# Performance work log

Measured on AMD Instinct MI355X. Metric: run time of the kernel, lower is better.

Reference implementation:

```python
import jax, jax.numpy as jnp
import numpy as np


def setup_inputs() -> dict:
    key = jax.random.key(0)
    k1, k2 = jax.random.split(key)
    x = jax.random.normal(k1, (32, 112, 112, 64), dtype=jnp.float32)
    kernels = jax.random.normal(k2, (3, 3, 64, 128), dtype=jnp.float32) * 0.05
    biases = jnp.zeros((128,), dtype=jnp.float32)
    return {"x": x, "kernels": kernels, "biases": biases}


def reference(x, kernels, biases):
    # Stride-1 VALID cross-correlation, NHWC input, HWIO kernel -> NHWC output.
    # Matches the original's per-pixel sum(patch * kernel) over all input channels.
    out = jax.lax.conv_general_dilated(
        x, kernels,
        window_strides=(1, 1),
        padding="VALID",
        dimension_numbers=("NHWC", "HWIO", "NHWC"),
    )
    out = out + biases  # broadcast over (B, H_out, W_out, F)
    return jax.nn.relu(out)  # activation=relu per init_kwargs
```

## Files before the change

### kernel.cpp

```cpp
#include <hip/hip_runtime.h>
#include <hip/hip_bf16.h>

typedef __attribute__((ext_vector_type(4))) float f32x4;
typedef __attribute__((ext_vector_type(8))) short bf16x8;
typedef __attribute__((ext_vector_type(8))) unsigned short u16x8;
typedef __attribute__((ext_vector_type(4))) unsigned int u32x4;

#define HH 112
#define WW 112
#define CIN 64
#define COUT 128
#define HOUT 110
#define WOUT 110
#define MTOT 387200
#define NWG 3025
#define NXCD 8

__device__ __forceinline__ unsigned short f2bf(float f) {
  unsigned int x = __float_as_uint(f);
  x += 0x7fffu + ((x >> 16) & 1u);
  return (unsigned short)(x >> 16);
}

__device__ __forceinline__ unsigned int cvt2(float lo, float hi) {
  union { __hip_bfloat162 h; unsigned int u; } cv;
  cv.h = __float22bfloat162_rn(float2{lo, hi});
  return cv.u;
}

__global__ void prepack_b_kernel(const float* __restrict__ kern,
                                 unsigned short* __restrict__ bt) {
  int idx = blockIdx.x * 256 + threadIdx.x;
  if (idx >= 576 * COUT) return;
  int co = idx / 576;
  int k = idx - co * 576;
  bt[idx] = f2bf(kern[k * COUT + co]);
}

template <bool PREPACK>
__global__ __launch_bounds__(512)
void conv_mfma_kernel(const float* __restrict__ x,
                      const void* __restrict__ bsrc,
                      const float* __restrict__ bias,
                      float* __restrict__ out) {
  __shared__ __align__(16) unsigned short As[2][128 * 64];
  __shared__ __align__(16) unsigned short Bs[2][128 * 64];

  const int tid = threadIdx.x;

  const int bid = blockIdx.x;
  const int q = NWG / NXCD, r = NWG % NXCD;
  const int xcd = bid % NXCD, i8 = bid / NXCD;
  const int wg = (xcd < r ? xcd * (q + 1) : r * (q + 1) + (xcd - r) * q) + i8;
  const int m0 = wg * 128;

  const int sr = tid >> 2;
  const int sc = tid & 3;
  const int m = m0 + sr;
  const int wo = m % WOUT;
  const int t1 = m / WOUT;
  const int ho = t1 % HOUT;
  const int b = t1 / HOUT;
  const float* xrow = x + (((b * HH) + ho) * WW + wo) * CIN + sc * 16;
  const int swzS = (sr & 7) << 4;
  const int awoff0 = sr * 64 + ((((sc * 32) + 0) ^ swzS) >> 1);
  const int awoff1 = sr * 64 + ((((sc * 32) + 16) ^ swzS) >> 1);

  const unsigned short* btrow = nullptr;
  if constexpr (PREPACK) {
    btrow = (const unsigned short*)bsrc + sr * 576 + sc * 16;
  }
  const int bci = tid >> 3;
  const int bco = (tid & 7) * 16;

  const int lane = tid & 63;
  const int wid = tid >> 6;
  const int wm = wid >> 1;
  const int wn = wid & 1;
  const int l16 = lane & 15;
  const int lk = lane >> 4;
  const int swzR = (l16 & 7) << 4;

  const int aroff0 = (wm * 32 + 0 + l16) * 64;
  const int aroff1 = (wm * 32 + 16 + l16) * 64;
  const int broff0 = (wn * 64 + 0 + l16) * 64;
  const int broff1 = (wn * 64 + 16 + l16) * 64;
  const int broff2 = (wn * 64 + 32 + l16) * 64;
  const int broff3 = (wn * 64 + 48 + l16) * 64;

  f32x4 acc[2][4];
#pragma unroll
  for (int i = 0; i < 2; ++i)
#pragma unroll
    for (int j = 0; j < 4; ++j)
      acc[i][j] = (f32x4){0.f, 0.f, 0.f, 0.f};

  {
    f32x4 f0 = *(const f32x4*)(xrow + 0);
    f32x4 f1 = *(const f32x4*)(xrow + 4);
    f32x4 f2 = *(const f32x4*)(xrow + 8);
    f32x4 f3 = *(const f32x4*)(xrow + 12);
    u32x4 va, vb;
    va[0] = cvt2(f0[0], f0[1]); va[1] = cvt2(f0[2], f0[3]);
    va[2] = cvt2(f1[0], f1[1]); va[3] = cvt2(f1[2], f1[3]);
    vb[0] = cvt2(f2[0], f2[1]); vb[1] = cvt2(f2[2], f2[3]);
    vb[2] = cvt2(f3[0], f3[1]); vb[3] = cvt2(f3[2], f3[3]);
    *(u32x4*)(As[0] + awoff0) = va;
    *(u32x4*)(As[0] + awoff1) = vb;
    if constexpr (PREPACK) {
      const u16x8* p = (const u16x8*)btrow;
      *(u16x8*)(Bs[0] + awoff0) = p[0];
      *(u16x8*)(Bs[0] + awoff1) = p[1];
    } else {
      const float* kern = (const float*)bsrc;
      const float* kslab = kern + bci * COUT + bco;
      f32x4 g0 = *(const f32x4*)(kslab + 0);
      f32x4 g1 = *(const f32x4*)(kslab + 4);
      f32x4 g2 = *(const f32x4*)(kslab + 8);
      f32x4 g3 = *(const f32x4*)(kslab + 12);
#pragma unroll
      for (int j = 0; j < 4; ++j) {
        int c0 = bco + j;
        Bs[0][c0 * 64 + (((bci * 2) ^ ((c0 & 7) << 4)) >> 1)] = f2bf(g0[j]);
        int c1 = bco + 4 + j;
        Bs[0][c1 * 64 + (((bci * 2) ^ ((c1 & 7) << 4)) >> 1)] = f2bf(g1[j]);
        int c2 = bco + 8 + j;
        Bs[0][c2 * 64 + (((bci * 2) ^ ((c2 & 7) << 4)) >> 1)] = f2bf(g2[j]);
        int c3 = bco + 12 + j;
        Bs[0][c3 * 64 + (((bci * 2) ^ ((c3 & 7) << 4)) >> 1)] = f2bf(g3[j]);
      }
    }
  }

#pragma unroll
  for (int kk = 0; kk < 9; ++kk) {
    const int cur = kk & 1;
    const int nxt = cur ^ 1;

    f32x4 g0, g1, g2, g3;
    u16x8 bq0, bq1;
    if (kk < 8) {
      const int kn = kk + 1;
      const int kh2 = kn / 3;
      const int kw2 = kn - kh2 * 3;
      const float* src = xrow + (kh2 * WW + kw2) * CIN;
      g0 = *(const f32x4*)(src + 0);
      g1 = *(const f32x4*)(src + 4);
      g2 = *(const f32x4*)(src + 8);
      g3 = *(const f32x4*)(src + 12);
      if constexpr (PREPACK) {
        const u16x8* p = (const u16x8*)(btrow + kn * 64);
        bq0 = p[0];
        bq1 = p[1];
      }
    }

    __syncthreads();

    const unsigned short* Ac = As[cur];
    const unsigned short* Bc = Bs[cur];
#pragma unroll
    for (int ks = 0; ks < 2; ++ks) {
      const int cbs = ((ks * 64 + lk * 16) ^ swzR) >> 1;
      bf16x8 a0 = *(const bf16x8*)(Ac + aroff0 + cbs);
      bf16x8 a1 = *(const bf16x8*)(Ac + aroff1 + cbs);
      bf16x8 b0 = *(const bf16x8*)(Bc + broff0 + cbs);
      bf16x8 b1 = *(const bf16x8*)(Bc + broff1 + cbs);
      bf16x8 b2 = *(const bf16x8*)(Bc + broff2 + cbs);
      bf16x8 b3 = *(const bf16x8*)(Bc + broff3 + cbs);
      acc[0][0] = __builtin_amdgcn_mfma_f32_16x16x32_bf16(a0, b0, acc[0][0], 0, 0, 0);
      acc[0][1] = __builtin_amdgcn_mfma_f32_16x16x32_bf16(a0, b1, acc[0][1], 0, 0, 0);
      acc[0][2] = __builtin_amdgcn_mfma_f32_16x16x32_bf16(a0, b2, acc[0][2], 0, 0, 0);
      acc[0][3] = __builtin_amdgcn_mfma_f32_16x16x32_bf16(a0, b3, acc[0][3], 0, 0, 0);
      acc[1][0] = __builtin_amdgcn_mfma_f32_16x16x32_bf16(a1, b0, acc[1][0], 0, 0, 0);
      acc[1][1] = __builtin_amdgcn_mfma_f32_16x16x32_bf16(a1, b1, acc[1][1], 0, 0, 0);
      acc[1][2] = __builtin_amdgcn_mfma_f32_16x16x32_bf16(a1, b2, acc[1][2], 0, 0, 0);
      acc[1][3] = __builtin_amdgcn_mfma_f32_16x16x32_bf16(a1, b3, acc[1][3], 0, 0, 0);
    }

    if (kk < 8) {
      u32x4 va, vb;
      va[0] = cvt2(g0[0], g0[1]); va[1] = cvt2(g0[2], g0[3]);
      va[2] = cvt2(g1[0], g1[1]); va[3] = cvt2(g1[2], g1[3]);
      vb[0] = cvt2(g2[0], g2[1]); vb[1] = cvt2(g2[2], g2[3]);
      vb[2] = cvt2(g3[0], g3[1]); vb[3] = cvt2(g3[2], g3[3]);
      *(u32x4*)(As[nxt] + awoff0) = va;
      *(u32x4*)(As[nxt] + awoff1) = vb;
      if constexpr (PREPACK) {
        *(u16x8*)(Bs[nxt] + awoff0) = bq0;
        *(u16x8*)(Bs[nxt] + awoff1) = bq1;
      } else {
        const float* kern = (const float*)bsrc;
        const float* kslab = kern + ((kk + 1) * 64 + bci) * COUT + bco;
        f32x4 h0 = *(const f32x4*)(kslab + 0);
        f32x4 h1 = *(const f32x4*)(kslab + 4);
        f32x4 h2 = *(const f32x4*)(kslab + 8);
        f32x4 h3 = *(const f32x4*)(kslab + 12);
#pragma unroll
        for (int j = 0; j < 4; ++j) {
          int c0 = bco + j;
          Bs[nxt][c0 * 64 + (((bci * 2) ^ ((c0 & 7) << 4)) >> 1)] = f2bf(h0[j]);
          int c1 = bco + 4 + j;
          Bs[nxt][c1 * 64 + (((bci * 2) ^ ((c1 & 7) << 4)) >> 1)] = f2bf(h1[j]);
          int c2 = bco + 8 + j;
          Bs[nxt][c2 * 64 + (((bci * 2) ^ ((c2 & 7) << 4)) >> 1)] = f2bf(h2[j]);
          int c3 = bco + 12 + j;
          Bs[nxt][c3 * 64 + (((bci * 2) ^ ((c3 & 7) << 4)) >> 1)] = f2bf(h3[j]);
        }
      }
    }
  }

  const int ncol = wn * 64 + l16;
  const float bv0 = bias[ncol + 0];
  const float bv1 = bias[ncol + 16];
  const float bv2 = bias[ncol + 32];
  const float bv3 = bias[ncol + 48];
  const int mrow0 = m0 + wm * 32 + lk * 4;
#pragma unroll
  for (int mf = 0; mf < 2; ++mf) {
#pragma unroll
    for (int j = 0; j < 4; ++j) {
      const int row = mrow0 + mf * 16 + j;
      float* orow = out + (size_t)row * COUT + ncol;
      orow[0]  = fmaxf(acc[mf][0][j] + bv0, 0.f);
      orow[16] = fmaxf(acc[mf][1][j] + bv1, 0.f);
      orow[32] = fmaxf(acc[mf][2][j] + bv2, 0.f);
      orow[48] = fmaxf(acc[mf][3][j] + bv3, 0.f);
    }
  }
}

extern "C" void kernel_launch(void* const* d_in, const int* in_sizes, int n_in,
                              void* d_out, int out_size, void* d_ws, size_t ws_size,
                              hipStream_t stream) {
  const float* x = (const float*)d_in[0];
  const float* kern = (const float*)d_in[1];
  const float* bias = (const float*)d_in[2];
  float* out = (float*)d_out;

  const size_t bt_bytes = 576 * COUT * sizeof(unsigned short);
  if (d_ws != nullptr && ws_size >= bt_bytes) {
    unsigned short* bt = (unsigned short*)d_ws;
    prepack_b_kernel<<<288, 256, 0, stream>>>(kern, bt);
    conv_mfma_kernel<true><<<NWG, 512, 0, stream>>>(x, (const void*)bt, bias, out);
  } else {
    conv_mfma_kernel<false><<<NWG, 512, 0, stream>>>(x, (const void*)kern, bias, out);
  }
}
```

Baseline: 118.1 us.

## Load A fragments directly from global into registers, drop A LDS staging

The im2col A operand no longer goes through shared memory. Each lane loads its MFMA fragment rows straight from global fp32 input, converts them to bf16 in registers, and prefetches the next tap. The weight prepack now writes into the already-swizzled LDS layout per tap, so staging B is a linear copy, and launch bounds request 4 blocks per CU. This removes LDS writes and reads for A and halves shared-memory use to raise occupancy, at the cost of redundant global loads, since the two waves sharing wm load the same A rows, and higher register pressure.

```diff
diff --git a/kernel.cpp b/kernel.cpp
--- a/kernel.cpp
+++ b/kernel.cpp
@@ -31,20 +31,22 @@
 __global__ void prepack_b_kernel(const float* __restrict__ kern,
                                  unsigned short* __restrict__ bt) {
   int idx = blockIdx.x * 256 + threadIdx.x;
-  if (idx >= 576 * COUT) return;
-  int co = idx / 576;
-  int k = idx - co * 576;
-  bt[idx] = f2bf(kern[k * COUT + co]);
+  if (idx >= 9 * 8192) return;
+  int tap = idx >> 13;
+  int rem = idx & 8191;
+  int co = rem >> 6;
+  int e = rem & 63;
+  int ci = ((e * 2) ^ ((co & 7) << 4)) >> 1;
+  bt[idx] = f2bf(kern[(tap * 64 + ci) * COUT + co]);
 }
 
 template <bool PREPACK>
-__global__ __launch_bounds__(512)
+__global__ __launch_bounds__(512, 4)
 void conv_mfma_kernel(const float* __restrict__ x,
                       const void* __restrict__ bsrc,
                       const float* __restrict__ bias,
                       float* __restrict__ out) {
-  __shared__ __align__(16) unsigned short As[2][128 * 64];
-  __shared__ __align__(16) unsigned short Bs[2][128 * 64];
+  __shared__ __align__(16) unsigned short Bs[2][8192];
 
   const int tid = threadIdx.x;
 
@@ -53,25 +55,6 @@
   const int xcd = bid % NXCD, i8 = bid / NXCD;
   const int wg = (xcd < r ? xcd * (q + 1) : r * (q + 1) + (xcd - r) * q) + i8;
   const int m0 = wg * 128;
-
-  const int sr = tid >> 2;
-  const int sc = tid & 3;
-  const int m = m0 + sr;
-  const int wo = m % WOUT;
-  const int t1 = m / WOUT;
-  const int ho = t1 % HOUT;
-  const int b = t1 / HOUT;
-  const float* xrow = x + (((b * HH) + ho) * WW + wo) * CIN + sc * 16;
-  const int swzS = (sr & 7) << 4;
-  const int awoff0 = sr * 64 + ((((sc * 32) + 0) ^ swzS) >> 1);
-  const int awoff1 = sr * 64 + ((((sc * 32) + 16) ^ swzS) >> 1);
-
-  const unsigned short* btrow = nullptr;
-  if constexpr (PREPACK) {
-    btrow = (const unsigned short*)bsrc + sr * 576 + sc * 16;
-  }
-  const int bci = tid >> 3;
-  const int bco = (tid & 7) * 16;
 
   const int lane = tid & 63;
   const int wid = tid >> 6;
@@ -81,8 +64,21 @@
   const int lk = lane >> 4;
   const int swzR = (l16 & 7) << 4;
 
-  const int aroff0 = (wm * 32 + 0 + l16) * 64;
-  const int aroff1 = (wm * 32 + 16 + l16) * 64;
+  const float* pa[2];
+#pragma unroll
+  for (int f = 0; f < 2; ++f) {
+    const int mrow = m0 + wm * 32 + f * 16 + l16;
+    const int wo = mrow % WOUT;
+    const int t = mrow / WOUT;
+    const int ho = t % HOUT;
+    const int bb = t / HOUT;
+    pa[f] = x + (((bb * HH) + ho) * WW + wo) * CIN + lk * 8;
+  }
+
+  const unsigned short* btp = (const unsigned short*)bsrc;
+  const int bci = tid >> 3;
+  const int bco = (tid & 7) * 16;
+
   const int broff0 = (wn * 64 + 0 + l16) * 64;
   const int broff1 = (wn * 64 + 16 + l16) * 64;
   const int broff2 = (wn * 64 + 32 + l16) * 64;
@@ -95,40 +91,27 @@
     for (int j = 0; j < 4; ++j)
       acc[i][j] = (f32x4){0.f, 0.f, 0.f, 0.f};
 
-  {
-    f32x4 f0 = *(const f32x4*)(xrow + 0);
-    f32x4 f1 = *(const f32x4*)(xrow + 4);
-    f32x4 f2 = *(const f32x4*)(xrow + 8);
-    f32x4 f3 = *(const f32x4*)(xrow + 12);
-    u32x4 va, vb;
-    va[0] = cvt2(f0[0], f0[1]); va[1] = cvt2(f0[2], f0[3]);
-    va[2] = cvt2(f1[0], f1[1]); va[3] = cvt2(f1[2], f1[3]);
-    vb[0] = cvt2(f2[0], f2[1]); vb[1] = cvt2(f2[2], f2[3]);
-    vb[2] = cvt2(f3[0], f3[1]); vb[3] = cvt2(f3[2], f3[3]);
-    *(u32x4*)(As[0] + awoff0) = va;
-    *(u32x4*)(As[0] + awoff1) = vb;
-    if constexpr (PREPACK) {
-      const u16x8* p = (const u16x8*)btrow;
-      *(u16x8*)(Bs[0] + awoff0) = p[0];
-      *(u16x8*)(Bs[0] + awoff1) = p[1];
-    } else {
-      const float* kern = (const float*)bsrc;
-      const float* kslab = kern + bci * COUT + bco;
-      f32x4 g0 = *(const f32x4*)(kslab + 0);
-      f32x4 g1 = *(const f32x4*)(kslab + 4);
-      f32x4 g2 = *(const f32x4*)(kslab + 8);
-      f32x4 g3 = *(const f32x4*)(kslab + 12);
-#pragma unroll
-      for (int j = 0; j < 4; ++j) {
-        int c0 = bco + j;
-        Bs[0][c0 * 64 + (((bci * 2) ^ ((c0 & 7) << 4)) >> 1)] = f2bf(g0[j]);
-        int c1 = bco + 4 + j;
-        Bs[0][c1 * 64 + (((bci * 2) ^ ((c1 & 7) << 4)) >> 1)] = f2bf(g1[j]);
-        int c2 = bco + 8 + j;
-        Bs[0][c2 * 64 + (((bci * 2) ^ ((c2 & 7) << 4)) >> 1)] = f2bf(g2[j]);
-        int c3 = bco + 12 + j;
-        Bs[0][c3 * 64 + (((bci * 2) ^ ((c3 & 7) << 4)) >> 1)] = f2bf(g3[j]);
-      }
+  f32x4 p[2][2][2];
+  u16x8 bq0, bq1;
+
+#pragma unroll
+  for (int f = 0; f < 2; ++f)
+#pragma unroll
+    for (int ks = 0; ks < 2; ++ks)
+#pragma unroll
+      for (int h = 0; h < 2; ++h)
+        p[f][ks][h] = *(const f32x4*)(pa[f] + ks * 32 + h * 4);
+  if constexpr (PREPACK) {
+    const u16x8* s = (const u16x8*)(btp + tid * 16);
+    *(u16x8*)(Bs[0] + tid * 16) = s[0];
+    *(u16x8*)(Bs[0] + tid * 16 + 8) = s[1];
+  } else {
+    const float* kern = (const float*)bsrc;
+    const float* kslab = kern + bci * COUT + bco;
+#pragma unroll
+    for (int j = 0; j < 16; ++j) {
+      int c = bco + j;
+      Bs[0][c * 64 + (((bci * 2) ^ ((c & 7) << 4)) >> 1)] = f2bf(kslab[j]);
     }
   }
 
@@ -137,75 +120,69 @@
     const int cur = kk & 1;
     const int nxt = cur ^ 1;
 
-    f32x4 g0, g1, g2, g3;
-    u16x8 bq0, bq1;
+    __syncthreads();
+
+    bf16x8 af[2][2];
+#pragma unroll
+    for (int f = 0; f < 2; ++f)
+#pragma unroll
+      for (int ks = 0; ks < 2; ++ks) {
+        union { u32x4 u; bf16x8 b; } cv;
+        cv.u[0] = cvt2(p[f][ks][0][0], p[f][ks][0][1]);
+        cv.u[1] = cvt2(p[f][ks][0][2], p[f][ks][0][3]);
+        cv.u[2] = cvt2(p[f][ks][1][0], p[f][ks][1][1]);
+        cv.u[3] = cvt2(p[f][ks][1][2], p[f][ks][1][3]);
+        af[f][ks] = cv.b;
+      }
+
     if (kk < 8) {
       const int kn = kk + 1;
       const int kh2 = kn / 3;
       const int kw2 = kn - kh2 * 3;
-      const float* src = xrow + (kh2 * WW + kw2) * CIN;
-      g0 = *(const f32x4*)(src + 0);
-      g1 = *(const f32x4*)(src + 4);
-      g2 = *(const f32x4*)(src + 8);
-      g3 = *(const f32x4*)(src + 12);
+      const int off = (kh2 * WW + kw2) * CIN;
+#pragma unroll
+      for (int f = 0; f < 2; ++f)
+#pragma unroll
+        for (int ks = 0; ks < 2; ++ks)
+#pragma unroll
+          for (int h = 0; h < 2; ++h)
+            p[f][ks][h] = *(const f32x4*)(pa[f] + off + ks * 32 + h * 4);
       if constexpr (PREPACK) {
-        const u16x8* p = (const u16x8*)(btrow + kn * 64);
-        bq0 = p[0];
-        bq1 = p[1];
+        const u16x8* s = (const u16x8*)(btp + kn * 8192 + tid * 16);
+        bq0 = s[0];
+        bq1 = s[1];
       }
     }
 
-    __syncthreads();
-
-    const unsigned short* Ac = As[cur];
     const unsigned short* Bc = Bs[cur];
 #pragma unroll
     for (int ks = 0; ks < 2; ++ks) {
       const int cbs = ((ks * 64 + lk * 16) ^ swzR) >> 1;
-      bf16x8 a0 = *(const bf16x8*)(Ac + aroff0 + cbs);
-      bf16x8 a1 = *(const bf16x8*)(Ac + aroff1 + cbs);
       bf16x8 b0 = *(const bf16x8*)(Bc + broff0 + cbs);
       bf16x8 b1 = *(const bf16x8*)(Bc + broff1 + cbs);
       bf16x8 b2 = *(const bf16x8*)(Bc + broff2 + cbs);
       bf16x8 b3 = *(const bf16x8*)(Bc + broff3 + cbs);
-      acc[0][0] = __builtin_amdgcn_mfma_f32_16x16x32_bf16(a0, b0, acc[0][0], 0, 0, 0);
-      acc[0][1] = __builtin_amdgcn_mfma_f32_16x16x32_bf16(a0, b1, acc[0][1], 0, 0, 0);
-      acc[0][2] = __builtin_amdgcn_mfma_f32_16x16x32_bf16(a0, b2, acc[0][2], 0, 0, 0);
-      acc[0][3] = __builtin_amdgcn_mfma_f32_16x16x32_bf16(a0, b3, acc[0][3], 0, 0, 0);
-      acc[1][0] = __builtin_amdgcn_mfma_f32_16x16x32_bf16(a1, b0, acc[1][0], 0, 0, 0);
-      acc[1][1] = __builtin_amdgcn_mfma_f32_16x16x32_bf16(a1, b1, acc[1][1], 0, 0, 0);
-      acc[1][2] = __builtin_amdgcn_mfma_f32_16x16x32_bf16(a1, b2, acc[1][2], 0, 0, 0);
-      acc[1][3] = __builtin_amdgcn_mfma_f32_16x16x32_bf16(a1, b3, acc[1][3], 0, 0, 0);
+      acc[0][0] = __builtin_amdgcn_mfma_f32_16x16x32_bf16(af[0][ks], b0, acc[0][0], 0, 0, 0);
+      acc[0][1] = __builtin_amdgcn_mfma_f32_16x16x32_bf16(af[0][ks], b1, acc[0][1], 0, 0, 0);
+      acc[0][2] = __builtin_amdgcn_mfma_f32_16x16x32_bf16(af[0][ks], b2, acc[0][2], 0, 0, 0);
+      acc[0][3] = __builtin_amdgcn_mfma_f32_16x16x32_bf16(af[0][ks], b3, acc[0][3], 0, 0, 0);
+      acc[1][0] = __builtin_amdgcn_mfma_f32_16x16x32_bf16(af[1][ks], b0, acc[1][0], 0, 0, 0);
+      acc[1][1] = __builtin_amdgcn_mfma_f32_16x16x32_bf16(af[1][ks], b1, acc[1][1], 0, 0, 0);
+      acc[1][2] = __builtin_amdgcn_mfma_f32_16x16x32_bf16(af[1][ks], b2, acc[1][2], 0, 0, 0);
+      acc[1][3] = __builtin_amdgcn_mfma_f32_16x16x32_bf16(af[1][ks], b3, acc[1][3], 0, 0, 0);
     }
 
     if (kk < 8) {
-      u32x4 va, vb;
-      va[0] = cvt2(g0[0], g0[1]); va[1] = cvt2(g0[2], g0[3]);
-      va[2] = cvt2(g1[0], g1[1]); va[3] = cvt2(g1[2], g1[3]);
-      vb[0] = cvt2(g2[0], g2[1]); vb[1] = cvt2(g2[2], g2[3]);
-      vb[2] = cvt2(g3[0], g3[1]); vb[3] = cvt2(g3[2], g3[3]);
-      *(u32x4*)(As[nxt] + awoff0) = va;
-      *(u32x4*)(As[nxt] + awoff1) = vb;
       if constexpr (PREPACK) {
-        *(u16x8*)(Bs[nxt] + awoff0) = bq0;
-        *(u16x8*)(Bs[nxt] + awoff1) = bq1;
+        *(u16x8*)(Bs[nxt] + tid * 16) = bq0;
+        *(u16x8*)(Bs[nxt] + tid * 16 + 8) = bq1;
       } else {
         const float* kern = (const float*)bsrc;
         const float* kslab = kern + ((kk + 1) * 64 + bci) * COUT + bco;
-        f32x4 h0 = *(const f32x4*)(kslab + 0);
-        f32x4 h1 = *(const f32x4*)(kslab + 4);
-        f32x4 h2 = *(const f32x4*)(kslab + 8);
-        f32x4 h3 = *(const f32x4*)(kslab + 12);
-#pragma unroll
-        for (int j = 0; j < 4; ++j) {
-          int c0 = bco + j;
-          Bs[nxt][c0 * 64 + (((bci * 2) ^ ((c0 & 7) << 4)) >> 1)] = f2bf(h0[j]);
-          int c1 = bco + 4 + j;
-          Bs[nxt][c1 * 64 + (((bci * 2) ^ ((c1 & 7) << 4)) >> 1)] = f2bf(h1[j]);
-          int c2 = bco + 8 + j;
-          Bs[nxt][c2 * 64 + (((bci * 2) ^ ((c2 & 7) << 4)) >> 1)] = f2bf(h2[j]);
-          int c3 = bco + 12 + j;
-          Bs[nxt][c3 * 64 + (((bci * 2) ^ ((c3 & 7) << 4)) >> 1)] = f2bf(h3[j]);
+#pragma unroll
+        for (int j = 0; j < 16; ++j) {
+          int c = bco + j;
+          Bs[nxt][c * 64 + (((bci * 2) ^ ((c & 7) << 4)) >> 1)] = f2bf(kslab[j]);
         }
       }
     }
@@ -239,7 +216,7 @@
   const float* bias = (const float*)d_in[2];
   float* out = (float*)d_out;
 
-  const size_t bt_bytes = 576 * COUT * sizeof(unsigned short);
+  const size_t bt_bytes = 9 * 8192 * sizeof(unsigned short);
   if (d_ws != nullptr && ws_size >= bt_bytes) {
     unsigned short* bt = (unsigned short*)d_ws;
     prepack_b_kernel<<<288, 256, 0, stream>>>(kern, bt);
```

New measurement: 229.6 us. 1.94x slower.

## Pre-convert input to bf16 and stream tiles into LDS via direct global-to-LDS loads

Applied to the files above, without the earlier changes.

Adds a pre-pass that converts the whole fp32 input to bf16 in workspace. It also prepacks weights per tap in the pre-swizzled LDS layout. The main conv kernel then fills A and B tiles with global_load_lds 16-byte DMA, which removes the register staging and the in-loop conversion, and drops one barrier per tap. The cost is an extra full read and write of the input (about 150MB of traffic) before the conv, which may outweigh the saved in-kernel work. It also requires a larger workspace; otherwise the code falls back to the old path.

```diff
diff --git a/kernel.cpp b/kernel.cpp
--- a/kernel.cpp
+++ b/kernel.cpp
@@ -15,6 +15,7 @@
 #define MTOT 387200
 #define NWG 3025
 #define NXCD 8
+#define XNE 25690112
 
 __device__ __forceinline__ unsigned short f2bf(float f) {
   unsigned int x = __float_as_uint(f);
@@ -28,25 +29,46 @@
   return cv.u;
 }
 
+__device__ __forceinline__ void gload16(const unsigned short* g, unsigned short* l) {
+  __builtin_amdgcn_global_load_lds(
+      (const __attribute__((address_space(1))) void*)g,
+      (__attribute__((address_space(3))) void*)l, 16, 0, 0);
+}
+
+__global__ __launch_bounds__(256)
+void cvt_x_kernel(const float* __restrict__ x, unsigned short* __restrict__ xb) {
+  const int t = blockIdx.x * 256 + threadIdx.x;
+  const f32x4* s = (const f32x4*)x + (size_t)t * 2;
+  f32x4 a = s[0], b = s[1];
+  u32x4 v;
+  v[0] = cvt2(a[0], a[1]); v[1] = cvt2(a[2], a[3]);
+  v[2] = cvt2(b[0], b[1]); v[3] = cvt2(b[2], b[3]);
+  ((u32x4*)xb)[t] = v;
+}
+
 __global__ void prepack_b_kernel(const float* __restrict__ kern,
                                  unsigned short* __restrict__ bt) {
   int idx = blockIdx.x * 256 + threadIdx.x;
-  if (idx >= 576 * COUT) return;
-  int co = idx / 576;
-  int k = idx - co * 576;
-  bt[idx] = f2bf(kern[k * COUT + co]);
-}
-
-template <bool PREPACK>
-__global__ __launch_bounds__(512)
-void conv_mfma_kernel(const float* __restrict__ x,
-                      const void* __restrict__ bsrc,
-                      const float* __restrict__ bias,
-                      float* __restrict__ out) {
-  __shared__ __align__(16) unsigned short As[2][128 * 64];
-  __shared__ __align__(16) unsigned short Bs[2][128 * 64];
+  if (idx >= 9 * 8192) return;
+  int tap = idx >> 13;
+  int rem = idx & 8191;
+  int co = rem >> 6;
+  int e = rem & 63;
+  int ci = ((e * 2) ^ ((co & 7) << 4)) >> 1;
+  bt[idx] = f2bf(kern[(tap * 64 + ci) * COUT + co]);
+}
+
+__global__ __launch_bounds__(512, 4)
+void conv_dma_kernel(const unsigned short* __restrict__ xb,
+                     const unsigned short* __restrict__ bt,
+                     const float* __restrict__ bias,
+                     float* __restrict__ out) {
+  __shared__ __align__(16) unsigned short As[2][8192];
+  __shared__ __align__(16) unsigned short Bs[2][8192];
 
   const int tid = threadIdx.x;
+  const int lane = tid & 63;
+  const int wid = tid >> 6;
 
   const int bid = blockIdx.x;
   const int q = NWG / NXCD, r = NWG % NXCD;
@@ -54,27 +76,26 @@
   const int wg = (xcd < r ? xcd * (q + 1) : r * (q + 1) + (xcd - r) * q) + i8;
   const int m0 = wg * 128;
 
-  const int sr = tid >> 2;
-  const int sc = tid & 3;
-  const int m = m0 + sr;
-  const int wo = m % WOUT;
-  const int t1 = m / WOUT;
-  const int ho = t1 % HOUT;
-  const int b = t1 / HOUT;
-  const float* xrow = x + (((b * HH) + ho) * WW + wo) * CIN + sc * 16;
-  const int swzS = (sr & 7) << 4;
-  const int awoff0 = sr * 64 + ((((sc * 32) + 0) ^ swzS) >> 1);
-  const int awoff1 = sr * 64 + ((((sc * 32) + 16) ^ swzS) >> 1);
-
-  const unsigned short* btrow = nullptr;
-  if constexpr (PREPACK) {
-    btrow = (const unsigned short*)bsrc + sr * 576 + sc * 16;
-  }
-  const int bci = tid >> 3;
-  const int bco = (tid & 7) * 16;
-
-  const int lane = tid & 63;
-  const int wid = tid >> 6;
+  int aoff[2];
+  const int obase = wid * 2048 + lane * 16;
+#pragma unroll
+  for (int j = 0; j < 2; ++j) {
+    const int o = obase + j * 1024;
+    const int rr = o >> 7;
+    const int ss = (o >> 4) & 7;
+    const int sp = ss ^ (rr & 7);
+    const int m = m0 + rr;
+    const int wo = m % WOUT;
+    const int t1 = m / WOUT;
+    const int ho = t1 % HOUT;
+    const int bb = t1 / HOUT;
+    aoff[j] = (((bb * HH) + ho) * WW + wo) * CIN + sp * 8;
+  }
+  const int ldsw0 = wid * 1024;
+  const int ldsw1 = wid * 1024 + 512;
+  const int blin0 = ldsw0 + lane * 8;
+  const int blin1 = ldsw1 + lane * 8;
+
   const int wm = wid >> 1;
   const int wn = wid & 1;
   const int l16 = lane & 15;
@@ -95,67 +116,28 @@
     for (int j = 0; j < 4; ++j)
       acc[i][j] = (f32x4){0.f, 0.f, 0.f, 0.f};
 
-  {
-    f32x4 f0 = *(const f32x4*)(xrow + 0);
-    f32x4 f1 = *(const f32x4*)(xrow + 4);
-    f32x4 f2 = *(const f32x4*)(xrow + 8);
-    f32x4 f3 = *(const f32x4*)(xrow + 12);
-    u32x4 va, vb;
-    va[0] = cvt2(f0[0], f0[1]); va[1] = cvt2(f0[2], f0[3]);
-    va[2] = cvt2(f1[0], f1[1]); va[3] = cvt2(f1[2], f1[3]);
-    vb[0] = cvt2(f2[0], f2[1]); vb[1] = cvt2(f2[2], f2[3]);
-    vb[2] = cvt2(f3[0], f3[1]); vb[3] = cvt2(f3[2], f3[3]);
-    *(u32x4*)(As[0] + awoff0) = va;
-    *(u32x4*)(As[0] + awoff1) = vb;
-    if constexpr (PREPACK) {
-      const u16x8* p = (const u16x8*)btrow;
-      *(u16x8*)(Bs[0] + awoff0) = p[0];
-      *(u16x8*)(Bs[0] + awoff1) = p[1];
-    } else {
-      const float* kern = (const float*)bsrc;
-      const float* kslab = kern + bci * COUT + bco;
-      f32x4 g0 = *(const f32x4*)(kslab + 0);
-      f32x4 g1 = *(const f32x4*)(kslab + 4);
-      f32x4 g2 = *(const f32x4*)(kslab + 8);
-      f32x4 g3 = *(const f32x4*)(kslab + 12);
-#pragma unroll
-      for (int j = 0; j < 4; ++j) {
-        int c0 = bco + j;
-        Bs[0][c0 * 64 + (((bci * 2) ^ ((c0 & 7) << 4)) >> 1)] = f2bf(g0[j]);
-        int c1 = bco + 4 + j;
-        Bs[0][c1 * 64 + (((bci * 2) ^ ((c1 & 7) << 4)) >> 1)] = f2bf(g1[j]);
-        int c2 = bco + 8 + j;
-        Bs[0][c2 * 64 + (((bci * 2) ^ ((c2 & 7) << 4)) >> 1)] = f2bf(g2[j]);
-        int c3 = bco + 12 + j;
-        Bs[0][c3 * 64 + (((bci * 2) ^ ((c3 & 7) << 4)) >> 1)] = f2bf(g3[j]);
-      }
-    }
-  }
+  gload16(xb + aoff[0], &As[0][ldsw0]);
+  gload16(xb + aoff[1], &As[0][ldsw1]);
+  gload16(bt + blin0, &Bs[0][ldsw0]);
+  gload16(bt + blin1, &Bs[0][ldsw1]);
+  __syncthreads();
 
 #pragma unroll
   for (int kk = 0; kk < 9; ++kk) {
     const int cur = kk & 1;
     const int nxt = cur ^ 1;
 
-    f32x4 g0, g1, g2, g3;
-    u16x8 bq0, bq1;
     if (kk < 8) {
       const int kn = kk + 1;
-      const int kh2 = kn / 3;
-      const int kw2 = kn - kh2 * 3;
-      const float* src = xrow + (kh2 * WW + kw2) * CIN;
-      g0 = *(const f32x4*)(src + 0);
-      g1 = *(const f32x4*)(src + 4);
-      g2 = *(const f32x4*)(src + 8);
-      g3 = *(const f32x4*)(src + 12);
-      if constexpr (PREPACK) {
-        const u16x8* p = (const u16x8*)(btrow + kn * 64);
-        bq0 = p[0];
-        bq1 = p[1];
-      }
-    }
-
-    __syncthreads();
+      const int kh = kn / 3;
+      const int kw = kn - kh * 3;
+      const int te = (kh * WW + kw) * CIN;
+      const int tb = kn * 8192;
+      gload16(xb + aoff[0] + te, &As[nxt][ldsw0]);
+      gload16(xb + aoff[1] + te, &As[nxt][ldsw1]);
+      gload16(bt + tb + blin0, &Bs[nxt][ldsw0]);
+      gload16(bt + tb + blin1, &Bs[nxt][ldsw1]);
+    }
 
     const unsigned short* Ac = As[cur];
     const unsigned short* Bc = Bs[cur];
@@ -178,6 +160,153 @@
       acc[1][3] = __builtin_amdgcn_mfma_f32_16x16x32_bf16(a1, b3, acc[1][3], 0, 0, 0);
     }
 
+    __syncthreads();
+  }
+
+  const int ncol = wn * 64 + l16;
+  const float bv0 = bias[ncol + 0];
+  const float bv1 = bias[ncol + 16];
+  const float bv2 = bias[ncol + 32];
+  const float bv3 = bias[ncol + 48];
+  const int mrow0 = m0 + wm * 32 + lk * 4;
+#pragma unroll
+  for (int mf = 0; mf < 2; ++mf) {
+#pragma unroll
+    for (int j = 0; j < 4; ++j) {
+      const int row = mrow0 + mf * 16 + j;
+      float* orow = out + (size_t)row * COUT + ncol;
+      orow[0]  = fmaxf(acc[mf][0][j] + bv0, 0.f);
+      orow[16] = fmaxf(acc[mf][1][j] + bv1, 0.f);
+      orow[32] = fmaxf(acc[mf][2][j] + bv2, 0.f);
+      orow[48] = fmaxf(acc[mf][3][j] + bv3, 0.f);
+    }
+  }
+}
+
+__global__ __launch_bounds__(512)
+void conv_fallback_kernel(const float* __restrict__ x,
+                          const float* __restrict__ kern,
+                          const float* __restrict__ bias,
+                          float* __restrict__ out) {
+  __shared__ __align__(16) unsigned short As[2][128 * 64];
+  __shared__ __align__(16) unsigned short Bs[2][128 * 64];
+
+  const int tid = threadIdx.x;
+  const int m0 = blockIdx.x * 128;
+
+  const int sr = tid >> 2;
+  const int sc = tid & 3;
+  const int m = m0 + sr;
+  const int wo = m % WOUT;
+  const int t1 = m / WOUT;
+  const int ho = t1 % HOUT;
+  const int b = t1 / HOUT;
+  const float* xrow = x + (((b * HH) + ho) * WW + wo) * CIN + sc * 16;
+  const int swzS = (sr & 7) << 4;
+  const int awoff0 = sr * 64 + ((((sc * 32) + 0) ^ swzS) >> 1);
+  const int awoff1 = sr * 64 + ((((sc * 32) + 16) ^ swzS) >> 1);
+
+  const int bci = tid >> 3;
+  const int bco = (tid & 7) * 16;
+
+  const int lane = tid & 63;
+  const int wid = tid >> 6;
+  const int wm = wid >> 1;
+  const int wn = wid & 1;
+  const int l16 = lane & 15;
+  const int lk = lane >> 4;
+  const int swzR = (l16 & 7) << 4;
+
+  const int aroff0 = (wm * 32 + 0 + l16) * 64;
+  const int aroff1 = (wm * 32 + 16 + l16) * 64;
+  const int broff0 = (wn * 64 + 0 + l16) * 64;
+  const int broff1 = (wn * 64 + 16 + l16) * 64;
+  const int broff2 = (wn * 64 + 32 + l16) * 64;
+  const int broff3 = (wn * 64 + 48 + l16) * 64;
+
+  f32x4 acc[2][4];
+#pragma unroll
+  for (int i = 0; i < 2; ++i)
+#pragma unroll
+    for (int j = 0; j < 4; ++j)
+      acc[i][j] = (f32x4){0.f, 0.f, 0.f, 0.f};
+
+  {
+    f32x4 f0 = *(const f32x4*)(xrow + 0);
+    f32x4 f1 = *(const f32x4*)(xrow + 4);
+    f32x4 f2 = *(const f32x4*)(xrow + 8);
+    f32x4 f3 = *(const f32x4*)(xrow + 12);
+    u32x4 va, vb;
+    va[0] = cvt2(f0[0], f0[1]); va[1] = cvt2(f0[2], f0[3]);
+    va[2] = cvt2(f1[0], f1[1]); va[3] = cvt2(f1[2], f1[3]);
+    vb[0] = cvt2(f2[0], f2[1]); vb[1] = cvt2(f2[2], f2[3]);
+    vb[2] = cvt2(f3[0], f3[1]); vb[3] = cvt2(f3[2], f3[3]);
+    *(u32x4*)(As[0] + awoff0) = va;
+    *(u32x4*)(As[0] + awoff1) = vb;
+    const float* kslab = kern + bci * COUT + bco;
+    f32x4 g0 = *(const f32x4*)(kslab + 0);
+    f32x4 g1 = *(const f32x4*)(kslab + 4);
+    f32x4 g2 = *(const f32x4*)(kslab + 8);
+    f32x4 g3 = *(const f32x4*)(kslab + 12);
+#pragma unroll
+    for (int j = 0; j < 4; ++j) {
+      int c0 = bco + j;
+      Bs[0][c0 * 64 + (((bci * 2) ^ ((c0 & 7) << 4)) >> 1)] = f2bf(g0[j]);
+      int c1 = bco + 4 + j;
+      Bs[0][c1 * 64 + (((bci * 2) ^ ((c1 & 7) << 4)) >> 1)] = f2bf(g1[j]);
+      int c2 = bco + 8 + j;
+      Bs[0][c2 * 64 + (((bci * 2) ^ ((c2 & 7) << 4)) >> 1)] = f2bf(g2[j]);
+      int c3 = bco + 12 + j;
+      Bs[0][c3 * 64 + (((bci * 2) ^ ((c3 & 7) << 4)) >> 1)] = f2bf(g3[j]);
+    }
+  }
+
+#pragma unroll
+  for (int kk = 0; kk < 9; ++kk) {
+    const int cur = kk & 1;
+    const int nxt = cur ^ 1;
+
+    f32x4 g0, g1, g2, g3;
+    f32x4 h0, h1, h2, h3;
+    if (kk < 8) {
+      const int kn = kk + 1;
+      const int kh2 = kn / 3;
+      const int kw2 = kn - kh2 * 3;
+      const float* src = xrow + (kh2 * WW + kw2) * CIN;
+      g0 = *(const f32x4*)(src + 0);
+      g1 = *(const f32x4*)(src + 4);
+      g2 = *(const f32x4*)(src + 8);
+      g3 = *(const f32x4*)(src + 12);
+      const float* kslab = kern + (kn * 64 + bci) * COUT + bco;
+      h0 = *(const f32x4*)(kslab + 0);
+      h1 = *(const f32x4*)(kslab + 4);
+      h2 = *(const f32x4*)(kslab + 8);
+      h3 = *(const f32x4*)(kslab + 12);
+    }
+
+    __syncthreads();
+
+    const unsigned short* Ac = As[cur];
+    const unsigned short* Bc = Bs[cur];
+#pragma unroll
+    for (int ks = 0; ks < 2; ++ks) {
+      const int cbs = ((ks * 64 + lk * 16) ^ swzR) >> 1;
+      bf16x8 a0 = *(const bf16x8*)(Ac + aroff0 + cbs);
+      bf16x8 a1 = *(const bf16x8*)(Ac + aroff1 + cbs);
+      bf16x8 b0 = *(const bf16x8*)(Bc + broff0 + cbs);
+      bf16x8 b1 = *(const bf16x8*)(Bc + broff1 + cbs);
+      bf16x8 b2 = *(const bf16x8*)(Bc + broff2 + cbs);
+      bf16x8 b3 = *(const bf16x8*)(Bc + broff3 + cbs);
+      acc[0][0] = __builtin_amdgcn_mfma_f32_16x16x32_bf16(a0, b0, acc[0][0], 0, 0, 0);
+      acc[0][1] = __builtin_amdgcn_mfma_f32_16x16x32_bf16(a0, b1, acc[0][1], 0, 0, 0);
+      acc[0][2] = __builtin_amdgcn_mfma_f32_16x16x32_bf16(a0, b2, acc[0][2], 0, 0, 0);
+      acc[0][3] = __builtin_amdgcn_mfma_f32_16x16x32_bf16(a0, b3, acc[0][3], 0, 0, 0);
+      acc[1][0] = __builtin_amdgcn_mfma_f32_16x16x32_bf16(a1, b0, acc[1][0], 0, 0, 0);
+      acc[1][1] = __builtin_amdgcn_mfma_f32_16x16x32_bf16(a1, b1, acc[1][1], 0, 0, 0);
+      acc[1][2] = __builtin_amdgcn_mfma_f32_16x16x32_bf16(a1, b2, acc[1][2], 0, 0, 0);
+      acc[1][3] = __builtin_amdgcn_mfma_f32_16x16x32_bf16(a1, b3, acc[1][3], 0, 0, 0);
+    }
+
     if (kk < 8) {
       u32x4 va, vb;
       va[0] = cvt2(g0[0], g0[1]); va[1] = cvt2(g0[2], g0[3]);
@@ -186,27 +315,16 @@
       vb[2] = cvt2(g3[0], g3[1]); vb[3] = cvt2(g3[2], g3[3]);
       *(u32x4*)(As[nxt] + awoff0) = va;
       *(u32x4*)(As[nxt] + awoff1) = vb;
-      if constexpr (PREPACK) {
-        *(u16x8*)(Bs[nxt] + awoff0) = bq0;
-        *(u16x8*)(Bs[nxt] + awoff1) = bq1;
-      } else {
-        const float* kern = (const float*)bsrc;
-        const float* kslab = kern + ((kk + 1) * 64 + bci) * COUT + bco;
-        f32x4 h0 = *(const f32x4*)(kslab + 0);
-        f32x4 h1 = *(const f32x4*)(kslab + 4);
-        f32x4 h2 = *(const f32x4*)(kslab + 8);
-        f32x4 h3 = *(const f32x4*)(kslab + 12);
-#pragma unroll
-        for (int j = 0; j < 4; ++j) {
-          int c0 = bco + j;
-          Bs[nxt][c0 * 64 + (((bci * 2) ^ ((c0 & 7) << 4)) >> 1)] = f2bf(h0[j]);
-          int c1 = bco + 4 + j;
-          Bs[nxt][c1 * 64 + (((bci * 2) ^ ((c1 & 7) << 4)) >> 1)] = f2bf(h1[j]);
-          int c2 = bco + 8 + j;
-          Bs[nxt][c2 * 64 + (((bci * 2) ^ ((c2 & 7) << 4)) >> 1)] = f2bf(h2[j]);
-          int c3 = bco + 12 + j;
-          Bs[nxt][c3 * 64 + (((bci * 2) ^ ((c3 & 7) << 4)) >> 1)] = f2bf(h3[j]);
-        }
+#pragma unroll
+      for (int j = 0; j < 4; ++j) {
+        int c0 = bco + j;
+        Bs[nxt][c0 * 64 + (((bci * 2) ^ ((c0 & 7) << 4)) >> 1)] = f2bf(h0[j]);
+        int c1 = bco + 4 + j;
+        Bs[nxt][c1 * 64 + (((bci * 2) ^ ((c1 & 7) << 4)) >> 1)] = f2bf(h1[j]);
+        int c2 = bco + 8 + j;
+        Bs[nxt][c2 * 64 + (((bci * 2) ^ ((c2 & 7) << 4)) >> 1)] = f2bf(h2[j]);
+        int c3 = bco + 12 + j;
+        Bs[nxt][c3 * 64 + (((bci * 2) ^ ((c3 & 7) << 4)) >> 1)] = f2bf(h3[j]);
       }
     }
   }
@@ -239,12 +357,15 @@
   const float* bias = (const float*)d_in[2];
   float* out = (float*)d_out;
 
-  const size_t bt_bytes = 576 * COUT * sizeof(unsigned short);
-  if (d_ws != nullptr && ws_size >= bt_bytes) {
-    unsigned short* bt = (unsigned short*)d_ws;
+  const size_t xb_bytes = (size_t)XNE * 2;
+  const size_t bt_bytes = 9 * 8192 * 2;
+  if (d_ws != nullptr && ws_size >= xb_bytes + bt_bytes) {
+    unsigned short* xb = (unsigned short*)d_ws;
+    unsigned short* bt = xb + XNE;
+    cvt_x_kernel<<<12544, 256, 0, stream>>>(x, xb);
     prepack_b_kernel<<<288, 256, 0, stream>>>(kern, bt);
-    conv_mfma_kernel<true><<<NWG, 512, 0, stream>>>(x, (const void*)bt, bias, out);
+    conv_dma_kernel<<<NWG, 512, 0, stream>>>(xb, bt, bias, out);
   } else {
-    conv_mfma_kernel<false><<<NWG, 512, 0, stream>>>(x, (const void*)kern, bias, out);
-  }
-}
+    conv_fallback_kernel<<<NWG, 512, 0, stream>>>(x, kern, bias, out);
+  }
+}
```

After: 110.1 us. 6.8% less time.
